# Kernel optimization log

Hardware: AMD Instinct MI355X
Metric: run time of the kernel (lower is better)

Reference implementation:

```python
import jax, jax.numpy as jnp
import numpy as np

B, P, ENC = 128, 196, 2048   # batch, num_pixels (14x14), encoder_dim
A, H, E, V = 512, 512, 512, 10000  # attention_dim, hidden, embed, vocab
T = 20  # max decode length (lengths max = T+1)


def setup_inputs() -> dict:
    key = jax.random.key(0)
    ks = jax.random.split(key, 24)
    def rn(k, shape, scale=0.05):
        return jax.random.normal(k, shape, jnp.float32) * scale
    encoder_out = jax.random.normal(ks[0], (B, P, ENC), jnp.float32)
    captions = jax.random.randint(ks[1], (B, T + 1), 0, V)
    # lengths sorted descending (packed-sequence convention), max forced to T+1
    lengths = jnp.sort(jax.random.randint(ks[2], (B,), 2, T + 2))[::-1]
    lengths = lengths.at[0].set(T + 1)
    return {
        "encoder_out": encoder_out,
        "captions": captions,
        "lengths": lengths,
        "W_enc_att": rn(ks[3], (A, ENC)), "b_enc_att": jnp.zeros((A,), jnp.float32),
        "W_dec_att": rn(ks[4], (A, H)),   "b_dec_att": jnp.zeros((A,), jnp.float32),
        "w_full_att": rn(ks[5], (1, A)),  "b_full_att": jnp.zeros((1,), jnp.float32),
        "emb_table": rn(ks[6], (V, E)),
        "W_ih": rn(ks[7], (4 * H, E + ENC)), "b_ih": jnp.zeros((4 * H,), jnp.float32),
        "W_hh": rn(ks[8], (4 * H, H)),       "b_hh": jnp.zeros((4 * H,), jnp.float32),
        "W_init_h": rn(ks[9], (H, ENC)),  "b_init_h": jnp.zeros((H,), jnp.float32),
        "W_init_c": rn(ks[10], (H, ENC)), "b_init_c": jnp.zeros((H,), jnp.float32),
        "W_fbeta": rn(ks[11], (ENC, H)),  "b_fbeta": jnp.zeros((ENC,), jnp.float32),
        "W_fc": rn(ks[12], (V, H)),       "b_fc": jnp.zeros((V,), jnp.float32),
    }


def reference(encoder_out, captions, lengths,
              W_enc_att, b_enc_att, W_dec_att, b_dec_att, w_full_att, b_full_att,
              emb_table, W_ih, b_ih, W_hh, b_hh,
              W_init_h, b_init_h, W_init_c, b_init_c,
              W_fbeta, b_fbeta, W_fc, b_fc):
    # Precompute encoder side of Bahdanau attention once (loop-invariant)
    att1 = jnp.einsum('bpe,ae->bpa', encoder_out, W_enc_att) + b_enc_att  # [B,P,A]
    emb = emb_table[captions]                                            # [B,T+1,E]
    mean_enc = encoder_out.mean(axis=1)                                  # [B,ENC]
    h0 = mean_enc @ W_init_h.T + b_init_h
    c0 = mean_enc @ W_init_c.T + b_init_c
    dec_len = lengths - 1
    # mask[t, b] = True while sample b still decodes at step t (== torch's b < batch_size_t for sorted lengths)
    mask = (jnp.arange(T)[:, None] < dec_len[None, :]).astype(encoder_out.dtype)  # [T,B]
    xs = (jnp.swapaxes(emb[:, :T, :], 0, 1), mask)  # ([T,B,E], [T,B])

    def step(carry, x):
        h, c = carry
        emb_t, m = x  # [B,E], [B]
        # Bahdanau attention
        att2 = h @ W_dec_att.T + b_dec_att                               # [B,A]
        e = jnp.einsum('bpa,a->bp', jax.nn.relu(att1 + att2[:, None, :]),
                       w_full_att[0]) + b_full_att[0]                    # [B,P]
        alpha = jax.nn.softmax(e, axis=1)
        context = jnp.einsum('bp,bpe->be', alpha, encoder_out)           # [B,ENC]
        gate = jax.nn.sigmoid(h @ W_fbeta.T + b_fbeta)
        context = gate * context
        # LSTMCell (PyTorch gate order: i, f, g, o); dropout is identity in eval mode
        x_in = jnp.concatenate([emb_t, context], axis=1)                 # [B,E+ENC]
        gates = x_in @ W_ih.T + b_ih + h @ W_hh.T + b_hh                 # [B,4H]
        i, f, g, o = jnp.split(gates, 4, axis=1)
        c_new = jax.nn.sigmoid(f) * c + jax.nn.sigmoid(i) * jnp.tanh(g)
        h_new = jax.nn.sigmoid(o) * jnp.tanh(c_new)
        pred = (h_new @ W_fc.T + b_fc) * m[:, None]                      # zeros past length
        mb = m[:, None]
        h = mb * h_new + (1.0 - mb) * h   # freeze state for finished rows
        c = mb * c_new + (1.0 - mb) * c
        return (h, c), pred

    (_, _), preds = jax.lax.scan(step, (h0, c0), xs)
    return jnp.swapaxes(preds, 0, 1)  # [B,T,V]
```

## Files before the change

kernel.cpp:

```cpp
#include <hip/hip_runtime.h>
#include <hip/hip_bf16.h>
#include <math.h>

#define B_   128
#define P_   196
#define ENC_ 2048
#define A_   512
#define H_   512
#define E_   512
#define V_   10000
#define T_   20
#define NDF_ 2560
#define XK_  3072
#define GK_  2560

typedef __attribute__((ext_vector_type(8))) short bf16x8;
typedef __attribute__((ext_vector_type(4))) short bf16x4;
typedef __attribute__((ext_vector_type(2))) short bf16x2;
typedef __attribute__((ext_vector_type(4))) float f32x4;

__device__ __forceinline__ float sigmoidf_(float x) { return 1.0f / (1.0f + expf(-x)); }

__device__ __forceinline__ short f2bf(float f) {
    unsigned u = __float_as_uint(f);
    u += 0x7fffu + ((u >> 16) & 1u);
    return (short)(u >> 16);
}
__device__ __forceinline__ float bf2f(short s) {
    return __uint_as_float(((unsigned)(unsigned short)s) << 16);
}
__device__ __forceinline__ void gload_lds16(const void* g, void* l) {
    __builtin_amdgcn_global_load_lds(
        (const __attribute__((address_space(1))) void*)g,
        (__attribute__((address_space(3))) void*)l, 16, 0, 0);
}

#define BM 128
#define BN 64
#define BK 64

#define COMPUTE64(ASP, BSP, CUR)                                               \
    _Pragma("unroll")                                                          \
    for (int kk = 0; kk < BK; kk += 32) {                                      \
        const int kb = (kk >> 3) + (lane >> 4);                                \
        bf16x8 av[4], bv[2];                                                   \
        _Pragma("unroll")                                                      \
        for (int i = 0; i < 4; i++) {                                          \
            int rr = wr * 64 + i * 16 + (lane & 15);                           \
            av[i] = *(const bf16x8*)&(ASP)[(CUR) * (BM * BK) + rr * BK         \
                    + ((kb ^ (rr & 7)) << 3)];                                 \
        }                                                                      \
        _Pragma("unroll")                                                      \
        for (int j = 0; j < 2; j++) {                                          \
            int cc = wc * 32 + j * 16 + (lane & 15);                           \
            bv[j] = *(const bf16x8*)&(BSP)[(CUR) * (BN * BK) + cc * BK         \
                    + ((kb ^ (cc & 7)) << 3)];                                 \
        }                                                                      \
        _Pragma("unroll")                                                      \
        for (int i = 0; i < 4; i++)                                            \
            _Pragma("unroll")                                                  \
            for (int j = 0; j < 2; j++)                                        \
                acc[i][j] = __builtin_amdgcn_mfma_f32_16x16x32_bf16(           \
                    av[i], bv[j], acc[i][j], 0, 0, 0);                         \
    }

__global__ __launch_bounds__(256) void gemm_bf(
    const short* __restrict__ A, const short* __restrict__ Bw,
    float* __restrict__ Cf, short* __restrict__ Cb,
    const float* __restrict__ bias,
    int N, int K, int lda, int ldb, int ldc,
    int mtiles, int ntiles, int pred,
    const int* __restrict__ lengths)
{
    __shared__ __attribute__((aligned(16))) short As[2][BM * BK];
    __shared__ __attribute__((aligned(16))) short Bs[2][BN * BK];
    int pm, pn;
    if (mtiles == 1) { pm = 0; pn = blockIdx.x; }
    else {
        int xcd = blockIdx.x & 7, s = blockIdx.x >> 3;
        pn = s % ntiles;
        pm = (s / ntiles) * 8 + xcd;
        if (pm >= mtiles) return;
    }
    const int bm = pm * BM, bn = pn * BN;
    const int tid = threadIdx.x, w = tid >> 6, lane = tid & 63;
    const int wr = w >> 1, wc = w & 1;
    const int lr8 = lane >> 3, lk = lane & 7;

    f32x4 zero4 = {0.f, 0.f, 0.f, 0.f};
    f32x4 acc[4][2];
    #pragma unroll
    for (int i = 0; i < 4; i++)
        #pragma unroll
        for (int j = 0; j < 2; j++) acc[i][j] = zero4;

#define STAGE(buf, k0) {                                                        \
    _Pragma("unroll")                                                           \
    for (int i = 0; i < 4; i++) {                                               \
        int row0 = w * 32 + i * 8; int row = row0 + lr8;                        \
        gload_lds16(A + (size_t)(bm + row) * lda + (k0)                         \
                    + ((lk ^ (row & 7)) << 3), &As[buf][row0 * BK]);            \
    }                                                                           \
    _Pragma("unroll")                                                           \
    for (int i = 0; i < 2; i++) {                                               \
        int row0 = w * 16 + i * 8; int row = row0 + lr8;                        \
        int gn = bn + row; if (gn > N - 1) gn = N - 1;                          \
        gload_lds16(Bw + (size_t)gn * ldb + (k0)                                \
                    + ((lk ^ (row & 7)) << 3), &Bs[buf][row0 * BK]);            \
    } }

    STAGE(0, 0);
    __syncthreads();
    int cur = 0;
    for (int k0 = 0; k0 < K; k0 += BK) {
        if (k0 + BK < K) STAGE(cur ^ 1, k0 + BK);
        COMPUTE64(&As[0][0], &Bs[0][0], cur);
        __syncthreads();
        cur ^= 1;
    }
#undef STAGE

    const int lr = lane >> 4, lc = lane & 15;
    #pragma unroll
    for (int i = 0; i < 4; i++) {
        #pragma unroll
        for (int r = 0; r < 4; r++) {
            int row = bm + wr * 64 + i * 16 + lr * 4 + r;
            #pragma unroll
            for (int j = 0; j < 2; j++) {
                int col = bn + wc * 32 + j * 16 + lc;
                if (col >= N) continue;
                float v = acc[i][j][r] + bias[col];
                if (pred) {
                    int tt = row >> 7, bb = row & 127;
                    float rs = (tt < lengths[bb] - 1) ? 1.0f : 0.0f;
                    Cf[(size_t)bb * T_ * V_ + (size_t)tt * V_ + col] = v * rs;
                } else if (Cb) {
                    Cb[(size_t)row * ldc + col] = f2bf(v);
                } else {
                    Cf[(size_t)row * ldc + col] = v;
                }
            }
        }
    }
}

__global__ __launch_bounds__(512) void esmctx_kernel(
    const short* __restrict__ att1_bf, const float* __restrict__ attf,
    const float* __restrict__ wfull, const short* __restrict__ enc_bf,
    short* __restrict__ ctxbuf, const int* __restrict__ lengths, int t)
{
    __shared__ float es[P_];
    __shared__ float red[256];
    __shared__ float al[P_];
    __shared__ float sm, ss;
    const int b = blockIdx.y, half = blockIdx.x;
    if (t >= lengths[b] - 1) return;
    const int tid = threadIdx.x, wv = tid >> 6, lane = tid & 63;

    float a2v[8], wv8[8];
    const float* a2 = attf + (size_t)b * NDF_;
    #pragma unroll
    for (int i = 0; i < 8; i++) {
        a2v[i] = a2[lane * 8 + i];
        wv8[i] = wfull[lane * 8 + i];
    }
    for (int row = wv; row < P_; row += 8) {
        bf16x8 a1 = *(const bf16x8*)(att1_bf + ((size_t)b * P_ + row) * A_ + lane * 8);
        float s = 0.0f;
        #pragma unroll
        for (int i = 0; i < 8; i++) {
            float v = bf2f(a1[i]) + a2v[i];
            s += fmaxf(v, 0.0f) * wv8[i];
        }
        #pragma unroll
        for (int off = 32; off > 0; off >>= 1) s += __shfl_down(s, off, 64);
        if (lane == 0) es[row] = s;
    }
    __syncthreads();
    float v = (tid < P_) ? es[tid] : -1e30f;
    if (tid < 256) red[tid] = v;
    __syncthreads();
    for (int rs = 128; rs > 0; rs >>= 1) {
        if (tid < rs) red[tid] = fmaxf(red[tid], red[tid + rs]);
        __syncthreads();
    }
    if (tid == 0) sm = red[0];
    __syncthreads();
    float ex = (tid < P_) ? expf(v - sm) : 0.0f;
    if (tid < 256) red[tid] = ex;
    __syncthreads();
    for (int rs = 128; rs > 0; rs >>= 1) {
        if (tid < rs) red[tid] += red[tid + rs];
        __syncthreads();
    }
    if (tid == 0) ss = red[0];
    __syncthreads();
    if (tid < P_) al[tid] = ex / ss;
    __syncthreads();

    const int c0 = half * 1024 + tid * 2;
    const short* eb = enc_bf + (size_t)b * P_ * ENC_ + c0;
    float s0 = 0, s1 = 0;
    for (int p = 0; p < P_; p++) {
        bf16x2 ev = *(const bf16x2*)(eb + (size_t)p * ENC_);
        float a = al[p];
        s0 += a * bf2f(ev[0]); s1 += a * bf2f(ev[1]);
    }
    const float* fb = attf + (size_t)b * NDF_ + A_;
    bf16x2 o;
    o[0] = f2bf(sigmoidf_(fb[c0 + 0]) * s0);
    o[1] = f2bf(sigmoidf_(fb[c0 + 1]) * s1);
    *(bf16x2*)(ctxbuf + (size_t)b * ENC_ + c0) = o;
}

__global__ __launch_bounds__(256) void gates_lstm(
    const short* __restrict__ ctxbuf, const short* __restrict__ hcur,
    short* __restrict__ hnxt,
    const short* __restrict__ Wcat, const float* __restrict__ gpre,
    float* __restrict__ cbuf, short* __restrict__ hn_t,
    const int* __restrict__ lengths, int t)
{
    __shared__ __attribute__((aligned(16))) char smem[49152];
    short* As0 = (short*)smem;
    short* Bs0 = (short*)(smem + 32768);
    const int bn = blockIdx.x * BN;
    const int tid = threadIdx.x, w = tid >> 6, lane = tid & 63;
    const int wr = w >> 1, wc = w & 1;
    const int lr8 = lane >> 3, lk = lane & 7;

    f32x4 zero4 = {0.f, 0.f, 0.f, 0.f};
    f32x4 acc[4][2];
    #pragma unroll
    for (int i = 0; i < 4; i++)
        #pragma unroll
        for (int j = 0; j < 2; j++) acc[i][j] = zero4;

#define STAGE_G(buf, k0) {                                                      \
    const short* Ap; int Al, kk0;                                               \
    if ((k0) < ENC_) { Ap = ctxbuf; Al = ENC_; kk0 = (k0); }                    \
    else             { Ap = hcur;   Al = H_;   kk0 = (k0) - ENC_; }             \
    _Pragma("unroll")                                                           \
    for (int i = 0; i < 4; i++) {                                               \
        int row0 = w * 32 + i * 8; int row = row0 + lr8;                        \
        gload_lds16(Ap + (size_t)row * Al + kk0 + ((lk ^ (row & 7)) << 3),      \
                    &As0[(buf) * (BM * BK) + row0 * BK]);                       \
    }                                                                           \
    _Pragma("unroll")                                                           \
    for (int i = 0; i < 2; i++) {                                               \
        int row0 = w * 16 + i * 8; int row = row0 + lr8;                        \
        gload_lds16(Wcat + (size_t)(bn + row) * XK_ + E_ + (k0)                 \
                    + ((lk ^ (row & 7)) << 3),                                  \
                    &Bs0[(buf) * (BN * BK) + row0 * BK]);                       \
    } }

    STAGE_G(0, 0);
    __syncthreads();
    int cur = 0;
    for (int k0 = 0; k0 < GK_; k0 += BK) {
        if (k0 + BK < GK_) STAGE_G(cur ^ 1, k0 + BK);
        COMPUTE64(As0, Bs0, cur);
        __syncthreads();
        cur ^= 1;
    }
#undef STAGE_G

    float* gl = (float*)smem;
    const int lr = lane >> 4, lc = lane & 15;
    #pragma unroll
    for (int i = 0; i < 4; i++)
        #pragma unroll
        for (int r = 0; r < 4; r++) {
            int row = wr * 64 + i * 16 + lr * 4 + r;
            #pragma unroll
            for (int j = 0; j < 2; j++) {
                int col = wc * 32 + j * 16 + lc;
                gl[row * 68 + col] = acc[i][j][r] + gpre[(size_t)row * (4 * H_) + bn + col];
            }
        }
    __syncthreads();
    #pragma unroll
    for (int q = 0; q < 8; q++) {
        int id  = tid * 8 + q;
        int row = id >> 4;
        int j   = id & 15;
        int jg  = (bn >> 2) + j;
        float i_ = sigmoidf_(gl[row * 68 + 4 * j + 0]);
        float f_ = sigmoidf_(gl[row * 68 + 4 * j + 1]);
        float g_ = tanhf    (gl[row * 68 + 4 * j + 2]);
        float o_ = sigmoidf_(gl[row * 68 + 4 * j + 3]);
        float cn = f_ * cbuf[row * H_ + jg] + i_ * g_;
        float hv = o_ * tanhf(cn);
        hn_t[row * H_ + jg] = f2bf(hv);
        bool m = t < lengths[row] - 1;
        if (m) cbuf[row * H_ + jg] = cn;
        hnxt[row * H_ + jg] = m ? f2bf(hv) : hcur[row * H_ + jg];
    }
}


__global__ __launch_bounds__(256) void castenc(const float* __restrict__ in,
                                               short* __restrict__ out)
{
    size_t i8 = ((size_t)blockIdx.x * 256 + threadIdx.x) * 8;
    float4 f0 = *(const float4*)(in + i8);
    float4 f1 = *(const float4*)(in + i8 + 4);
    bf16x8 v;
    v[0] = f2bf(f0.x); v[1] = f2bf(f0.y); v[2] = f2bf(f0.z); v[3] = f2bf(f0.w);
    v[4] = f2bf(f1.x); v[5] = f2bf(f1.y); v[6] = f2bf(f1.z); v[7] = f2bf(f1.w);
    *(bf16x8*)(out + i8) = v;
}

__global__ __launch_bounds__(256) void castk(const float* __restrict__ in,
                                             short* __restrict__ out, int n)
{
    int i4 = (blockIdx.x * 256 + threadIdx.x) * 4;
    if (i4 >= n) return;
    float4 f = *(const float4*)(in + i4);
    out[i4 + 0] = f2bf(f.x); out[i4 + 1] = f2bf(f.y);
    out[i4 + 2] = f2bf(f.z); out[i4 + 3] = f2bf(f.w);
}

__global__ __launch_bounds__(256) void wdf_kernel(const float* __restrict__ W_dec,
                                                  const float* __restrict__ W_fbeta,
                                                  short* __restrict__ out)
{
    int k = blockIdx.x * 256 + threadIdx.x;
    int n = blockIdx.y;
    float v = (n < A_) ? W_dec[(size_t)n * H_ + k]
                       : W_fbeta[(size_t)(n - A_) * H_ + k];
    out[(size_t)n * H_ + k] = f2bf(v);
}

__global__ __launch_bounds__(256) void wcat_kernel(const float* __restrict__ W_ih,
                                                   const float* __restrict__ W_hh,
                                                   short* __restrict__ out)
{
    int k = blockIdx.x * 256 + threadIdx.x;
    int n = blockIdx.y;
    int srow = (n & 3) * H_ + (n >> 2);
    float v = (k < E_ + ENC_) ? W_ih[(size_t)srow * (E_ + ENC_) + k]
                              : W_hh[(size_t)srow * H_ + (k - (E_ + ENC_))];
    out[(size_t)n * XK_ + k] = f2bf(v);
}

__global__ __launch_bounds__(256) void bdf_kernel(const float* __restrict__ b_dec,
                                                  const float* __restrict__ b_fbeta,
                                                  float* __restrict__ out)
{
    int j = blockIdx.x * 256 + threadIdx.x;
    if (j < NDF_) out[j] = (j < A_) ? b_dec[j] : b_fbeta[j - A_];
}

__global__ __launch_bounds__(256) void bcat_kernel(const float* __restrict__ b_ih,
                                                   const float* __restrict__ b_hh,
                                                   float* __restrict__ out)
{
    int j = blockIdx.x * 256 + threadIdx.x;
    if (j < 4 * H_) {
        int srow = (j & 3) * H_ + (j >> 2);
        out[j] = b_ih[srow] + b_hh[srow];
    }
}

__global__ __launch_bounds__(256) void mean_kernel(const short* __restrict__ enc_bf,
                                                   short* __restrict__ meanE_bf)
{
    int g = blockIdx.x * 256 + threadIdx.x;
    int b = g >> 8, cb = g & 255;
    const short* p = enc_bf + (size_t)b * P_ * ENC_ + cb * 8;
    float s[8] = {};
    for (int i = 0; i < P_; i++) {
        bf16x8 v = *(const bf16x8*)(p + (size_t)i * ENC_);
        #pragma unroll
        for (int j = 0; j < 8; j++) s[j] += bf2f(v[j]);
    }
    bf16x8 o;
    #pragma unroll
    for (int j = 0; j < 8; j++) o[j] = f2bf(s[j] * (1.0f / (float)P_));
    *(bf16x8*)(meanE_bf + (size_t)b * ENC_ + cb * 8) = o;
}

__global__ __launch_bounds__(256) void emball_kernel(const int* __restrict__ captions,
                                                     const float* __restrict__ table,
                                                     short* __restrict__ emb_all)
{
    int idx = blockIdx.x * 256 + threadIdx.x;
    int col = idx & 511;
    int bt  = idx >> 9;
    int b   = bt & 127;
    int t   = bt >> 7;
    int tok = captions[b * (T_ + 1) + t];
    emb_all[(size_t)t * B_ * E_ + (size_t)b * E_ + col] = f2bf(table[(size_t)tok * E_ + col]);
}

extern "C" void kernel_launch(void* const* d_in, const int* in_sizes, int n_in,
                              void* d_out, int out_size, void* d_ws, size_t ws_size,
                              hipStream_t stream)
{
    const float* enc      = (const float*)d_in[0];
    const int*   captions = (const int*)  d_in[1];
    const int*   lengths  = (const int*)  d_in[2];
    const float* W_enc    = (const float*)d_in[3];
    const float* b_enc    = (const float*)d_in[4];
    const float* W_dec    = (const float*)d_in[5];
    const float* b_dec    = (const float*)d_in[6];
    const float* w_full   = (const float*)d_in[7];
    const float* emb_tab  = (const float*)d_in[9];
    const float* W_ih     = (const float*)d_in[10];
    const float* b_ih     = (const float*)d_in[11];
    const float* W_hh     = (const float*)d_in[12];
    const float* b_hh     = (const float*)d_in[13];
    const float* W_init_h = (const float*)d_in[14];
    const float* b_init_h = (const float*)d_in[15];
    const float* W_init_c = (const float*)d_in[16];
    const float* b_init_c = (const float*)d_in[17];
    const float* W_fbeta  = (const float*)d_in[18];
    const float* b_fbeta  = (const float*)d_in[19];
    const float* W_fc     = (const float*)d_in[20];
    const float* b_fc     = (const float*)d_in[21];
    float* out = (float*)d_out;

    char* ws = (char*)d_ws;
    size_t off = 0;
    auto alloc = [&](size_t bytes) { void* p = ws + off; off += (bytes + 255) & ~(size_t)255; return p; };
    short* enc_bf    = (short*)alloc((size_t)B_ * P_ * ENC_ * 2);
    short* att1_bf   = (short*)alloc((size_t)B_ * P_ * A_ * 2);
    short* Wenc_bf   = (short*)alloc((size_t)A_ * ENC_ * 2);
    short* Wih_bf    = (short*)alloc((size_t)H_ * ENC_ * 2);
    short* Wic_bf    = (short*)alloc((size_t)H_ * ENC_ * 2);
    short* Wdf_bf    = (short*)alloc((size_t)NDF_ * H_ * 2);
    short* Wcat_bf   = (short*)alloc((size_t)4 * H_ * XK_ * 2);
    short* Wfc_bf    = (short*)alloc((size_t)V_ * H_ * 2);
    float* bdf       = (float*)alloc(NDF_ * 4);
    float* bcat      = (float*)alloc(4 * H_ * 4);
    short* meanE_bf  = (short*)alloc((size_t)B_ * ENC_ * 2);
    float* cbuf      = (float*)alloc((size_t)B_ * H_ * 4);
    short* hbufs     = (short*)alloc((size_t)2 * B_ * H_ * 2);
    short* emb_all   = (short*)alloc((size_t)T_ * B_ * E_ * 2);
    short* hn_all    = (short*)alloc((size_t)T_ * B_ * H_ * 2);
    float* attf      = (float*)alloc((size_t)B_ * NDF_ * 4);
    short* ctxbuf    = (short*)alloc((size_t)B_ * ENC_ * 2);
    float* gates_pre = (float*)alloc((size_t)T_ * B_ * 4 * H_ * 4);
    (void)ws_size;

    castenc<<<(B_ * P_ * ENC_) / (256 * 8), 256, 0, stream>>>(enc, enc_bf);
    castk<<<(A_ * ENC_ / 4 + 255) / 256, 256, 0, stream>>>(W_enc, Wenc_bf, A_ * ENC_);
    castk<<<(H_ * ENC_ / 4 + 255) / 256, 256, 0, stream>>>(W_init_h, Wih_bf, H_ * ENC_);
    castk<<<(H_ * ENC_ / 4 + 255) / 256, 256, 0, stream>>>(W_init_c, Wic_bf, H_ * ENC_);
    castk<<<(V_ * H_ / 4 + 255) / 256, 256, 0, stream>>>(W_fc, Wfc_bf, V_ * H_);
    wdf_kernel<<<dim3(H_ / 256, NDF_), 256, 0, stream>>>(W_dec, W_fbeta, Wdf_bf);
    wcat_kernel<<<dim3(XK_ / 256, 4 * H_), 256, 0, stream>>>(W_ih, W_hh, Wcat_bf);
    bdf_kernel<<<(NDF_ + 255) / 256, 256, 0, stream>>>(b_dec, b_fbeta, bdf);
    bcat_kernel<<<(4 * H_ + 255) / 256, 256, 0, stream>>>(b_ih, b_hh, bcat);
    mean_kernel<<<(B_ * ENC_ / 8) / 256, 256, 0, stream>>>(enc_bf, meanE_bf);
    emball_kernel<<<(T_ * B_ * E_) / 256, 256, 0, stream>>>(captions, emb_tab, emb_all);

    gemm_bf<<<8 * 8 * ((196 + 7) / 8), 256, 0, stream>>>(
        enc_bf, Wenc_bf, nullptr, att1_bf, b_enc,
        A_, ENC_, ENC_, ENC_, A_, 196, 8, 0, nullptr);
    gemm_bf<<<8 * 32 * (((T_ * B_) / BM + 7) / 8), 256, 0, stream>>>(
        emb_all, Wcat_bf, gates_pre, nullptr, bcat,
        4 * H_, E_, E_, XK_, 4 * H_, (T_ * B_) / BM, 32, 0, nullptr);
    gemm_bf<<<H_ / BN, 256, 0, stream>>>(
        meanE_bf, Wih_bf, nullptr, hbufs, b_init_h,
        H_, ENC_, ENC_, ENC_, H_, 1, H_ / BN, 0, nullptr);
    gemm_bf<<<H_ / BN, 256, 0, stream>>>(
        meanE_bf, Wic_bf, cbuf, nullptr, b_init_c,
        H_, ENC_, ENC_, ENC_, H_, 1, H_ / BN, 0, nullptr);

    for (int t = 0; t < T_; t++) {
        short* hcur = hbufs + (size_t)(t & 1) * B_ * H_;
        short* hnxt = hbufs + (size_t)((t & 1) ^ 1) * B_ * H_;
        gemm_bf<<<NDF_ / BN, 256, 0, stream>>>(
            hcur, Wdf_bf, attf, nullptr, bdf,
            NDF_, H_, H_, H_, NDF_, 1, NDF_ / BN, 0, nullptr);
        esmctx_kernel<<<dim3(2, B_), 512, 0, stream>>>(
            att1_bf, attf, w_full, enc_bf, ctxbuf, lengths, t);
        gates_lstm<<<(4 * H_) / BN, 256, 0, stream>>>(
            ctxbuf, hcur, hnxt, Wcat_bf, gates_pre + (size_t)t * B_ * 4 * H_,
            cbuf, hn_all + (size_t)t * B_ * H_, lengths, t);
    }
    gemm_bf<<<8 * 157 * (((T_ * B_) / BM + 7) / 8), 256, 0, stream>>>(
        hn_all, Wfc_bf, out, nullptr, b_fc,
        V_, H_, H_, H_, 0, (T_ * B_) / BM, 157, 1, lengths);
}
```

Baseline: 1.839 ms.

## Fuse decoder attention projection into attention kernel and merge prep kernels

Removes the per-step GEMM that computed the decoder attention projection and the f_beta gate. Each attention block now computes those dot products itself from h held in LDS, so every block of each batch row re-reads the Wdf weights (2.6 MB) with scalar FMA instead of MFMA. Separately, the many setup cast kernels are merged into one prep kernel, the encoder cast is fused with the mean, and the two init GEMMs are merged into one launch. This cuts the launch count, but the recomputed weight reads are redundant and could cost more than the removed GEMM.

```diff
diff --git a/kernel.cpp b/kernel.cpp
--- a/kernel.cpp
+++ b/kernel.cpp
@@ -69,7 +69,7 @@
     float* __restrict__ Cf, short* __restrict__ Cb,
     const float* __restrict__ bias,
     int N, int K, int lda, int ldb, int ldc,
-    int mtiles, int ntiles, int pred,
+    int mtiles, int ntiles, int mode,
     const int* __restrict__ lengths)
 {
     __shared__ __attribute__((aligned(16))) short As[2][BM * BK];
@@ -131,10 +131,13 @@
                 int col = bn + wc * 32 + j * 16 + lc;
                 if (col >= N) continue;
                 float v = acc[i][j][r] + bias[col];
-                if (pred) {
+                if (mode == 1) {
                     int tt = row >> 7, bb = row & 127;
                     float rs = (tt < lengths[bb] - 1) ? 1.0f : 0.0f;
                     Cf[(size_t)bb * T_ * V_ + (size_t)tt * V_ + col] = v * rs;
+                } else if (mode == 2) {
+                    if (col < H_) Cb[(size_t)row * H_ + col] = f2bf(v);
+                    else          Cf[(size_t)row * H_ + (col - H_)] = v;
                 } else if (Cb) {
                     Cb[(size_t)row * ldc + col] = f2bf(v);
                 } else {
@@ -145,27 +148,44 @@
     }
 }
 
-__global__ __launch_bounds__(512) void esmctx_kernel(
-    const short* __restrict__ att1_bf, const float* __restrict__ attf,
+__global__ __launch_bounds__(512) void attesm_kernel(
+    const short* __restrict__ att1_bf, const short* __restrict__ hcur,
+    const short* __restrict__ Wdf, const float* __restrict__ bdf,
     const float* __restrict__ wfull, const short* __restrict__ enc_bf,
     short* __restrict__ ctxbuf, const int* __restrict__ lengths, int t)
 {
+    __shared__ float h_lds[512];
+    __shared__ float als[512];
     __shared__ float es[P_];
     __shared__ float red[256];
     __shared__ float al[P_];
     __shared__ float sm, ss;
     const int b = blockIdx.y, half = blockIdx.x;
     if (t >= lengths[b] - 1) return;
-    const int tid = threadIdx.x, wv = tid >> 6, lane = tid & 63;
+    const int tid = threadIdx.x, w = tid >> 6, lane = tid & 63;
+
+    h_lds[tid] = bf2f(hcur[(size_t)b * H_ + tid]);
+    __syncthreads();
+
+    {
+        const short* wrow = Wdf + (size_t)tid * H_;
+        float acc = bdf[tid];
+        for (int k8 = 0; k8 < H_ / 8; k8++) {
+            bf16x8 wv = *(const bf16x8*)(wrow + k8 * 8);
+            #pragma unroll
+            for (int i = 0; i < 8; i++) acc += h_lds[k8 * 8 + i] * bf2f(wv[i]);
+        }
+        als[tid] = acc;
+    }
+    __syncthreads();
 
     float a2v[8], wv8[8];
-    const float* a2 = attf + (size_t)b * NDF_;
     #pragma unroll
     for (int i = 0; i < 8; i++) {
-        a2v[i] = a2[lane * 8 + i];
+        a2v[i] = als[lane * 8 + i];
         wv8[i] = wfull[lane * 8 + i];
     }
-    for (int row = wv; row < P_; row += 8) {
+    for (int row = w; row < P_; row += 8) {
         bf16x8 a1 = *(const bf16x8*)(att1_bf + ((size_t)b * P_ + row) * A_ + lane * 8);
         float s = 0.0f;
         #pragma unroll
@@ -200,6 +220,23 @@
     __syncthreads();
 
     const int c0 = half * 1024 + tid * 2;
+    float g0 = bdf[A_ + c0], g1 = bdf[A_ + c0 + 1];
+    {
+        const short* w0 = Wdf + (size_t)(A_ + c0) * H_;
+        const short* w1 = w0 + H_;
+        for (int k8 = 0; k8 < H_ / 8; k8++) {
+            bf16x8 v0 = *(const bf16x8*)(w0 + k8 * 8);
+            bf16x8 v1 = *(const bf16x8*)(w1 + k8 * 8);
+            #pragma unroll
+            for (int i = 0; i < 8; i++) {
+                float hv = h_lds[k8 * 8 + i];
+                g0 += hv * bf2f(v0[i]);
+                g1 += hv * bf2f(v1[i]);
+            }
+        }
+        g0 = sigmoidf_(g0);
+        g1 = sigmoidf_(g1);
+    }
     const short* eb = enc_bf + (size_t)b * P_ * ENC_ + c0;
     float s0 = 0, s1 = 0;
     for (int p = 0; p < P_; p++) {
@@ -207,10 +244,9 @@
         float a = al[p];
         s0 += a * bf2f(ev[0]); s1 += a * bf2f(ev[1]);
     }
-    const float* fb = attf + (size_t)b * NDF_ + A_;
     bf16x2 o;
-    o[0] = f2bf(sigmoidf_(fb[c0 + 0]) * s0);
-    o[1] = f2bf(sigmoidf_(fb[c0 + 1]) * s1);
+    o[0] = f2bf(g0 * s0);
+    o[1] = f2bf(g1 * s1);
     *(bf16x2*)(ctxbuf + (size_t)b * ENC_ + c0) = o;
 }
 
@@ -298,100 +334,119 @@
     }
 }
 
-
-__global__ __launch_bounds__(256) void castenc(const float* __restrict__ in,
-                                               short* __restrict__ out)
+__global__ __launch_bounds__(256) void castenc_mean(const float* __restrict__ enc,
+                                                    short* __restrict__ enc_bf,
+                                                    short* __restrict__ meanE_bf)
 {
-    size_t i8 = ((size_t)blockIdx.x * 256 + threadIdx.x) * 8;
-    float4 f0 = *(const float4*)(in + i8);
-    float4 f1 = *(const float4*)(in + i8 + 4);
-    bf16x8 v;
-    v[0] = f2bf(f0.x); v[1] = f2bf(f0.y); v[2] = f2bf(f0.z); v[3] = f2bf(f0.w);
-    v[4] = f2bf(f1.x); v[5] = f2bf(f1.y); v[6] = f2bf(f1.z); v[7] = f2bf(f1.w);
-    *(bf16x8*)(out + i8) = v;
-}
-
-__global__ __launch_bounds__(256) void castk(const float* __restrict__ in,
-                                             short* __restrict__ out, int n)
+    const int b = blockIdx.y;
+    const int c0 = blockIdx.x * 1024 + threadIdx.x * 4;
+    const float* src = enc + (size_t)b * P_ * ENC_ + c0;
+    short* dst = enc_bf + (size_t)b * P_ * ENC_ + c0;
+    float s0 = 0, s1 = 0, s2 = 0, s3 = 0;
+    for (int p = 0; p < P_; p++) {
+        float4 f = *(const float4*)(src + (size_t)p * ENC_);
+        bf16x4 v;
+        v[0] = f2bf(f.x); v[1] = f2bf(f.y); v[2] = f2bf(f.z); v[3] = f2bf(f.w);
+        *(bf16x4*)(dst + (size_t)p * ENC_) = v;
+        s0 += f.x; s1 += f.y; s2 += f.z; s3 += f.w;
+    }
+    const float inv = 1.0f / (float)P_;
+    bf16x4 m;
+    m[0] = f2bf(s0 * inv); m[1] = f2bf(s1 * inv);
+    m[2] = f2bf(s2 * inv); m[3] = f2bf(s3 * inv);
+    *(bf16x4*)(meanE_bf + (size_t)b * ENC_ + c0) = m;
+}
+
+#define PB0 1024
+#define PB1 (PB0 + 2048)
+#define PB2 (PB1 + 5000)
+#define PB3 (PB2 + 1280)
+#define PB4 (PB3 + 6144)
+#define PB5 (PB4 + 1280)
+#define PB6 (PB5 + 3)
+#define PB7 (PB6 + 2)
+#define PB8 (PB7 + 1)
+
+__device__ __forceinline__ void cast4(const float* __restrict__ in,
+                                      short* __restrict__ out, int i4) {
+    float4 f = *(const float4*)(in + i4);
+    bf16x4 v;
+    v[0] = f2bf(f.x); v[1] = f2bf(f.y); v[2] = f2bf(f.z); v[3] = f2bf(f.w);
+    *(bf16x4*)(out + i4) = v;
+}
+__device__ __forceinline__ void cast4p(const float* __restrict__ src,
+                                       short* __restrict__ out, int i4) {
+    float4 f = *(const float4*)src;
+    bf16x4 v;
+    v[0] = f2bf(f.x); v[1] = f2bf(f.y); v[2] = f2bf(f.z); v[3] = f2bf(f.w);
+    *(bf16x4*)(out + i4) = v;
+}
+
+__global__ __launch_bounds__(256) void prep_kernel(
+    const float* __restrict__ W_enc,    const float* __restrict__ W_init_h,
+    const float* __restrict__ W_init_c, const float* __restrict__ W_fc,
+    const float* __restrict__ W_dec,    const float* __restrict__ W_fbeta,
+    const float* __restrict__ W_ih,     const float* __restrict__ W_hh,
+    const int*   __restrict__ captions, const float* __restrict__ emb_tab,
+    const float* __restrict__ b_dec,    const float* __restrict__ b_fbeta,
+    const float* __restrict__ b_ih,     const float* __restrict__ b_hh,
+    const float* __restrict__ b_init_h, const float* __restrict__ b_init_c,
+    short* __restrict__ Wenc_bf,  short* __restrict__ Winit_bf,
+    short* __restrict__ Wfc_bf,   short* __restrict__ Wdf_bf,
+    short* __restrict__ Wcat_bf,  short* __restrict__ emb_all,
+    float* __restrict__ bdf,      float* __restrict__ bcat,
+    float* __restrict__ binit)
 {
-    int i4 = (blockIdx.x * 256 + threadIdx.x) * 4;
-    if (i4 >= n) return;
-    float4 f = *(const float4*)(in + i4);
-    out[i4 + 0] = f2bf(f.x); out[i4 + 1] = f2bf(f.y);
-    out[i4 + 2] = f2bf(f.z); out[i4 + 3] = f2bf(f.w);
-}
-
-__global__ __launch_bounds__(256) void wdf_kernel(const float* __restrict__ W_dec,
-                                                  const float* __restrict__ W_fbeta,
-                                                  short* __restrict__ out)
-{
-    int k = blockIdx.x * 256 + threadIdx.x;
-    int n = blockIdx.y;
-    float v = (n < A_) ? W_dec[(size_t)n * H_ + k]
-                       : W_fbeta[(size_t)(n - A_) * H_ + k];
-    out[(size_t)n * H_ + k] = f2bf(v);
-}
-
-__global__ __launch_bounds__(256) void wcat_kernel(const float* __restrict__ W_ih,
-                                                   const float* __restrict__ W_hh,
-                                                   short* __restrict__ out)
-{
-    int k = blockIdx.x * 256 + threadIdx.x;
-    int n = blockIdx.y;
-    int srow = (n & 3) * H_ + (n >> 2);
-    float v = (k < E_ + ENC_) ? W_ih[(size_t)srow * (E_ + ENC_) + k]
-                              : W_hh[(size_t)srow * H_ + (k - (E_ + ENC_))];
-    out[(size_t)n * XK_ + k] = f2bf(v);
-}
-
-__global__ __launch_bounds__(256) void bdf_kernel(const float* __restrict__ b_dec,
-                                                  const float* __restrict__ b_fbeta,
-                                                  float* __restrict__ out)
-{
-    int j = blockIdx.x * 256 + threadIdx.x;
-    if (j < NDF_) out[j] = (j < A_) ? b_dec[j] : b_fbeta[j - A_];
-}
-
-__global__ __launch_bounds__(256) void bcat_kernel(const float* __restrict__ b_ih,
-                                                   const float* __restrict__ b_hh,
-                                                   float* __restrict__ out)
-{
-    int j = blockIdx.x * 256 + threadIdx.x;
-    if (j < 4 * H_) {
-        int srow = (j & 3) * H_ + (j >> 2);
-        out[j] = b_ih[srow] + b_hh[srow];
-    }
-}
-
-__global__ __launch_bounds__(256) void mean_kernel(const short* __restrict__ enc_bf,
-                                                   short* __restrict__ meanE_bf)
-{
-    int g = blockIdx.x * 256 + threadIdx.x;
-    int b = g >> 8, cb = g & 255;
-    const short* p = enc_bf + (size_t)b * P_ * ENC_ + cb * 8;
-    float s[8] = {};
-    for (int i = 0; i < P_; i++) {
-        bf16x8 v = *(const bf16x8*)(p + (size_t)i * ENC_);
-        #pragma unroll
-        for (int j = 0; j < 8; j++) s[j] += bf2f(v[j]);
-    }
-    bf16x8 o;
-    #pragma unroll
-    for (int j = 0; j < 8; j++) o[j] = f2bf(s[j] * (1.0f / (float)P_));
-    *(bf16x8*)(meanE_bf + (size_t)b * ENC_ + cb * 8) = o;
-}
-
-__global__ __launch_bounds__(256) void emball_kernel(const int* __restrict__ captions,
-                                                     const float* __restrict__ table,
-                                                     short* __restrict__ emb_all)
-{
-    int idx = blockIdx.x * 256 + threadIdx.x;
-    int col = idx & 511;
-    int bt  = idx >> 9;
-    int b   = bt & 127;
-    int t   = bt >> 7;
-    int tok = captions[b * (T_ + 1) + t];
-    emb_all[(size_t)t * B_ * E_ + (size_t)b * E_ + col] = f2bf(table[(size_t)tok * E_ + col]);
+    const int blk = blockIdx.x, tid = threadIdx.x;
+    if (blk < PB0) {
+        cast4(W_enc, Wenc_bf, blk * 1024 + tid * 4);
+    } else if (blk < PB1) {
+        int i4 = (blk - PB0) * 1024 + tid * 4;
+        int n = i4 >> 11, k = i4 & 2047;
+        const float* src = (n < H_) ? W_init_h + (size_t)n * ENC_ + k
+                                    : W_init_c + (size_t)(n - H_) * ENC_ + k;
+        cast4p(src, Winit_bf, i4);
+    } else if (blk < PB2) {
+        cast4(W_fc, Wfc_bf, (blk - PB1) * 1024 + tid * 4);
+    } else if (blk < PB3) {
+        int i4 = (blk - PB2) * 1024 + tid * 4;
+        int n = i4 >> 9, k = i4 & 511;
+        const float* src = (n < A_) ? W_dec + (size_t)n * H_ + k
+                                    : W_fbeta + (size_t)(n - A_) * H_ + k;
+        cast4p(src, Wdf_bf, i4);
+    } else if (blk < PB4) {
+        int i4 = (blk - PB3) * 1024 + tid * 4;
+        int n = i4 / XK_, k = i4 - n * XK_;
+        int srow = (n & 3) * H_ + (n >> 2);
+        const float* src = (k < E_ + ENC_) ? W_ih + (size_t)srow * (E_ + ENC_) + k
+                                           : W_hh + (size_t)srow * H_ + (k - (E_ + ENC_));
+        cast4p(src, Wcat_bf, i4);
+    } else if (blk < PB5) {
+        int i4 = (blk - PB4) * 1024 + tid * 4;
+        int col = i4 & 511;
+        int bt  = i4 >> 9;
+        int b   = bt & 127;
+        int tt  = bt >> 7;
+        int tok = captions[b * (T_ + 1) + tt];
+        cast4p(emb_tab + (size_t)tok * E_ + col, emb_all, i4);
+    } else if (blk < PB6) {
+        int j = (blk - PB5) * 1024 + tid * 4;
+        #pragma unroll
+        for (int q = 0; q < 4; q++, j++)
+            if (j < NDF_) bdf[j] = (j < A_) ? b_dec[j] : b_fbeta[j - A_];
+    } else if (blk < PB7) {
+        int j = (blk - PB6) * 1024 + tid * 4;
+        #pragma unroll
+        for (int q = 0; q < 4; q++, j++) {
+            int srow = (j & 3) * H_ + (j >> 2);
+            bcat[j] = b_ih[srow] + b_hh[srow];
+        }
+    } else {
+        int j = tid * 4;
+        #pragma unroll
+        for (int q = 0; q < 4; q++, j++)
+            binit[j] = (j < H_) ? b_init_h[j] : b_init_c[j - H_];
+    }
 }
 
 extern "C" void kernel_launch(void* const* d_in, const int* in_sizes, int n_in,
@@ -427,34 +482,27 @@
     short* enc_bf    = (short*)alloc((size_t)B_ * P_ * ENC_ * 2);
     short* att1_bf   = (short*)alloc((size_t)B_ * P_ * A_ * 2);
     short* Wenc_bf   = (short*)alloc((size_t)A_ * ENC_ * 2);
-    short* Wih_bf    = (short*)alloc((size_t)H_ * ENC_ * 2);
-    short* Wic_bf    = (short*)alloc((size_t)H_ * ENC_ * 2);
+    short* Winit_bf  = (short*)alloc((size_t)2 * H_ * ENC_ * 2);
     short* Wdf_bf    = (short*)alloc((size_t)NDF_ * H_ * 2);
     short* Wcat_bf   = (short*)alloc((size_t)4 * H_ * XK_ * 2);
     short* Wfc_bf    = (short*)alloc((size_t)V_ * H_ * 2);
     float* bdf       = (float*)alloc(NDF_ * 4);
     float* bcat      = (float*)alloc(4 * H_ * 4);
+    float* binit     = (float*)alloc(2 * H_ * 4);
     short* meanE_bf  = (short*)alloc((size_t)B_ * ENC_ * 2);
     float* cbuf      = (float*)alloc((size_t)B_ * H_ * 4);
     short* hbufs     = (short*)alloc((size_t)2 * B_ * H_ * 2);
     short* emb_all   = (short*)alloc((size_t)T_ * B_ * E_ * 2);
     short* hn_all    = (short*)alloc((size_t)T_ * B_ * H_ * 2);
-    float* attf      = (float*)alloc((size_t)B_ * NDF_ * 4);
     short* ctxbuf    = (short*)alloc((size_t)B_ * ENC_ * 2);
     float* gates_pre = (float*)alloc((size_t)T_ * B_ * 4 * H_ * 4);
     (void)ws_size;
 
-    castenc<<<(B_ * P_ * ENC_) / (256 * 8), 256, 0, stream>>>(enc, enc_bf);
-    castk<<<(A_ * ENC_ / 4 + 255) / 256, 256, 0, stream>>>(W_enc, Wenc_bf, A_ * ENC_);
-    castk<<<(H_ * ENC_ / 4 + 255) / 256, 256, 0, stream>>>(W_init_h, Wih_bf, H_ * ENC_);
-    castk<<<(H_ * ENC_ / 4 + 255) / 256, 256, 0, stream>>>(W_init_c, Wic_bf, H_ * ENC_);
-    castk<<<(V_ * H_ / 4 + 255) / 256, 256, 0, stream>>>(W_fc, Wfc_bf, V_ * H_);
-    wdf_kernel<<<dim3(H_ / 256, NDF_), 256, 0, stream>>>(W_dec, W_fbeta, Wdf_bf);
-    wcat_kernel<<<dim3(XK_ / 256, 4 * H_), 256, 0, stream>>>(W_ih, W_hh, Wcat_bf);
-    bdf_kernel<<<(NDF_ + 255) / 256, 256, 0, stream>>>(b_dec, b_fbeta, bdf);
-    bcat_kernel<<<(4 * H_ + 255) / 256, 256, 0, stream>>>(b_ih, b_hh, bcat);
-    mean_kernel<<<(B_ * ENC_ / 8) / 256, 256, 0, stream>>>(enc_bf, meanE_bf);
-    emball_kernel<<<(T_ * B_ * E_) / 256, 256, 0, stream>>>(captions, emb_tab, emb_all);
+    prep_kernel<<<PB8, 256, 0, stream>>>(
+        W_enc, W_init_h, W_init_c, W_fc, W_dec, W_fbeta, W_ih, W_hh,
+        captions, emb_tab, b_dec, b_fbeta, b_ih, b_hh, b_init_h, b_init_c,
+        Wenc_bf, Winit_bf, Wfc_bf, Wdf_bf, Wcat_bf, emb_all, bdf, bcat, binit);
+    castenc_mean<<<dim3(2, B_), 256, 0, stream>>>(enc, enc_bf, meanE_bf);
 
     gemm_bf<<<8 * 8 * ((196 + 7) / 8), 256, 0, stream>>>(
         enc_bf, Wenc_bf, nullptr, att1_bf, b_enc,
@@ -462,21 +510,15 @@
     gemm_bf<<<8 * 32 * (((T_ * B_) / BM + 7) / 8), 256, 0, stream>>>(
         emb_all, Wcat_bf, gates_pre, nullptr, bcat,
         4 * H_, E_, E_, XK_, 4 * H_, (T_ * B_) / BM, 32, 0, nullptr);
-    gemm_bf<<<H_ / BN, 256, 0, stream>>>(
-        meanE_bf, Wih_bf, nullptr, hbufs, b_init_h,
-        H_, ENC_, ENC_, ENC_, H_, 1, H_ / BN, 0, nullptr);
-    gemm_bf<<<H_ / BN, 256, 0, stream>>>(
-        meanE_bf, Wic_bf, cbuf, nullptr, b_init_c,
-        H_, ENC_, ENC_, ENC_, H_, 1, H_ / BN, 0, nullptr);
+    gemm_bf<<<(2 * H_) / BN, 256, 0, stream>>>(
+        meanE_bf, Winit_bf, cbuf, hbufs, binit,
+        2 * H_, ENC_, ENC_, ENC_, 0, 1, (2 * H_) / BN, 2, nullptr);
 
     for (int t = 0; t < T_; t++) {
         short* hcur = hbufs + (size_t)(t & 1) * B_ * H_;
         short* hnxt = hbufs + (size_t)((t & 1) ^ 1) * B_ * H_;
-        gemm_bf<<<NDF_ / BN, 256, 0, stream>>>(
-            hcur, Wdf_bf, attf, nullptr, bdf,
-            NDF_, H_, H_, H_, NDF_, 1, NDF_ / BN, 0, nullptr);
-        esmctx_kernel<<<dim3(2, B_), 512, 0, stream>>>(
-            att1_bf, attf, w_full, enc_bf, ctxbuf, lengths, t);
+        attesm_kernel<<<dim3(2, B_), 512, 0, stream>>>(
+            att1_bf, hcur, Wdf_bf, bdf, w_full, enc_bf, ctxbuf, lengths, t);
         gates_lstm<<<(4 * H_) / BN, 256, 0, stream>>>(
             ctxbuf, hcur, hnxt, Wcat_bf, gates_pre + (size_t)t * B_ * 4 * H_,
             cbuf, hn_all + (size_t)t * B_ * H_, lengths, t);
```

After: 2.461 ms. +33.8%, slower.
